# Performance work log

Hardware: AMD Instinct MI355X
Metric: run time of the kernel (lower is better)

## Reference

```python
import jax, jax.numpy as jnp
import numpy as np


def setup_inputs() -> dict:
    key = jax.random.key(0)
    k1, k2 = jax.random.split(key)
    shape = (64, 512, 512)  # batch of radar QPE grids
    # targets: rain rates uniform in [0, 100) so every weight bin is hit
    y = jax.random.uniform(k1, shape, dtype=jnp.float32) * 100.0
    # predictions: target plus noise -> realistic abs-diff magnitudes
    p = y + jax.random.normal(k2, shape, dtype=jnp.float32) * 5.0
    weights = jnp.array([0.1, 1.0, 2.0, 4.0, 8.0, 16.0, 32.0], dtype=jnp.float32)
    edge = jnp.array([0.0, 0.1, 10.0, 20.0, 30.0, 40.0, 50.0, 100.0], dtype=jnp.float32)
    return {"y": y, "p": p, "weights": weights, "edge": edge}


def reference(y, p, weights, edge):
    # diff = |p - y|
    diff = jnp.abs(p - y)
    # Fused bucketize replacing the 7-iteration mask+cat loop:
    # bin b satisfies edge[b] <= y < edge[b+1]  (searchsorted side='right' - 1)
    bin_idx = jnp.searchsorted(edge, y, side="right") - 1
    n_bins = weights.shape[0]
    valid = (bin_idx >= 0) & (bin_idx < n_bins)  # elements outside [edge[0], edge[-1]) are dropped
    w = jnp.where(valid, weights[jnp.clip(bin_idx, 0, n_bins - 1)], jnp.float32(0.0))
    total = jnp.sum(w * diff)
    count = jnp.sum(valid).astype(diff.dtype)  # len(loss_list) in the original
    return total / count
```

## Files before the change

kernel.cpp:

```cpp
#include <hip/hip_runtime.h>
#include <hip/hip_bf16.h>
#include <math.h>


#define MAXB 8
#define NBLOCKS 1024
#define BLOCK 256

__global__ __launch_bounds__(BLOCK) void wmae_partial(
    const float* __restrict__ y, const float* __restrict__ p,
    const float* __restrict__ weights, const float* __restrict__ edge,
    int n, int n_bins, int n_edges,
    float* __restrict__ psum, float* __restrict__ pcnt)
{
    __shared__ float sh_e[256];
    __shared__ float sh_w[256];
    for (int j = threadIdx.x; j < n_edges && j < 256; j += BLOCK) sh_e[j] = edge[j];
    for (int j = threadIdx.x; j < n_bins  && j < 256; j += BLOCK) sh_w[j] = weights[j];
    __syncthreads();

    float ev[MAXB], wv[MAXB];
#pragma unroll
    for (int j = 0; j < MAXB; ++j) {
        ev[j] = (j < n_edges) ? edge[j] : 3.4e38f;
        wv[j] = (j < n_bins)  ? weights[j] : 0.0f;
    }
    const float e0 = edge[0];
    const float eup = (n_bins < n_edges) ? edge[n_bins] : 3.4e38f;

    float sum = 0.0f;
    int   cnt = 0;

    auto proc = [&](float yy, float pp) {
        float w = 0.0f;
#pragma unroll
        for (int j = 0; j < MAXB; ++j) {
            if (j < n_bins) w = (yy >= ev[j]) ? wv[j] : w;
        }
        if (n_bins > MAXB) {
            for (int j = MAXB; j < n_bins; ++j)
                w = (yy >= sh_e[j]) ? sh_w[j] : w;
        }
        bool valid = (yy >= e0) && (yy < eup);
        sum += (valid ? w : 0.0f) * fabsf(pp - yy);
        cnt += valid ? 1 : 0;
    };

    const int tid    = blockIdx.x * BLOCK + threadIdx.x;
    const int stride = gridDim.x * BLOCK;
    const int n4     = n >> 2;
    const float4* y4 = (const float4*)y;
    const float4* p4 = (const float4*)p;

    for (int i = tid; i < n4; i += stride) {
        float4 yv = y4[i];
        float4 pv = p4[i];
        proc(yv.x, pv.x);
        proc(yv.y, pv.y);
        proc(yv.z, pv.z);
        proc(yv.w, pv.w);
    }
    for (int i = (n4 << 2) + tid; i < n; i += stride) proc(y[i], p[i]);

#pragma unroll
    for (int off = 32; off > 0; off >>= 1) {
        sum += __shfl_down(sum, off, 64);
        cnt += __shfl_down(cnt, off, 64);
    }
    __shared__ float wsum[BLOCK / 64];
    __shared__ int   wcnt[BLOCK / 64];
    const int wave = threadIdx.x >> 6;
    const int lane = threadIdx.x & 63;
    if (lane == 0) { wsum[wave] = sum; wcnt[wave] = cnt; }
    __syncthreads();
    if (threadIdx.x == 0) {
        float s = 0.0f; int c = 0;
#pragma unroll
        for (int w2 = 0; w2 < BLOCK / 64; ++w2) { s += wsum[w2]; c += wcnt[w2]; }
        psum[blockIdx.x] = s;
        pcnt[blockIdx.x] = (float)c;
    }
}

__global__ __launch_bounds__(BLOCK) void wmae_final(
    const float* __restrict__ psum, const float* __restrict__ pcnt,
    int nparts, float* __restrict__ out)
{
    float s = 0.0f, c = 0.0f;
    for (int i = threadIdx.x; i < nparts; i += BLOCK) { s += psum[i]; c += pcnt[i]; }
#pragma unroll
    for (int off = 32; off > 0; off >>= 1) {
        s += __shfl_down(s, off, 64);
        c += __shfl_down(c, off, 64);
    }
    __shared__ float wsum[BLOCK / 64];
    __shared__ float wcnt[BLOCK / 64];
    const int wave = threadIdx.x >> 6;
    const int lane = threadIdx.x & 63;
    if (lane == 0) { wsum[wave] = s; wcnt[wave] = c; }
    __syncthreads();
    if (threadIdx.x == 0) {
        float S = 0.0f, C = 0.0f;
#pragma unroll
        for (int w2 = 0; w2 < BLOCK / 64; ++w2) { S += wsum[w2]; C += wcnt[w2]; }
        out[0] = S / C;
    }
}

extern "C" void kernel_launch(void* const* d_in, const int* in_sizes, int n_in,
                              void* d_out, int out_size, void* d_ws, size_t ws_size,
                              hipStream_t stream) {
    const float* y       = (const float*)d_in[0];
    const float* p       = (const float*)d_in[1];
    const float* weights = (const float*)d_in[2];
    const float* edge    = (const float*)d_in[3];
    const int n       = in_sizes[0];
    const int n_bins  = in_sizes[2];
    const int n_edges = in_sizes[3];

    float* psum = (float*)d_ws;
    float* pcnt = psum + NBLOCKS;
    float* out  = (float*)d_out;

    wmae_partial<<<NBLOCKS, BLOCK, 0, stream>>>(y, p, weights, edge,
                                                n, n_bins, n_edges, psum, pcnt);
    wmae_final<<<1, BLOCK, 0, stream>>>(psum, pcnt, NBLOCKS, out);
}
```

Before: 148.7 us.

## Double-buffer per-wave chunk loads with inline asm and scalar-register bin tables

Replaces the grid-stride float4 loop with per-wave 4KB chunks loaded through inline-asm global_load_dwordx4, double-buffered so the next chunk's loads are in flight while the current one is computed, using explicit s_waitcnt. Edge and weight tables are forced into scalar registers via readfirstlane, the shared-memory copy is removed, and the bin loop no longer tests n_bins inside. The aim is more memory-level parallelism for this bandwidth-bound reduction. In exchange it doubles the live vector registers per thread and relies on hand-written waitcnt correctness.

After: 151.2 us. Within noise of the previous version (+1.7%).

```diff
diff --git a/kernel.cpp b/kernel.cpp
--- a/kernel.cpp
+++ b/kernel.cpp
@@ -4,8 +4,35 @@
 
 
 #define MAXB 8
-#define NBLOCKS 1024
+#define NB   1024
 #define BLOCK 256
+
+typedef float vf4 __attribute__((ext_vector_type(4)));
+
+__device__ __forceinline__ float to_sgpr(float x) {
+    return __uint_as_float(__builtin_amdgcn_readfirstlane(__float_as_uint(x)));
+}
+
+#define ISSUE(Y0,Y1,Y2,Y3,P0,P1,P2,P3, YB, PB)                                      \
+    asm volatile("global_load_dwordx4 %0, %1, off"             : "=v"(Y0) : "v"(YB)); \
+    asm volatile("global_load_dwordx4 %0, %1, off offset:1024" : "=v"(Y1) : "v"(YB)); \
+    asm volatile("global_load_dwordx4 %0, %1, off offset:2048" : "=v"(Y2) : "v"(YB)); \
+    asm volatile("global_load_dwordx4 %0, %1, off offset:3072" : "=v"(Y3) : "v"(YB)); \
+    asm volatile("global_load_dwordx4 %0, %1, off"             : "=v"(P0) : "v"(PB)); \
+    asm volatile("global_load_dwordx4 %0, %1, off offset:1024" : "=v"(P1) : "v"(PB)); \
+    asm volatile("global_load_dwordx4 %0, %1, off offset:2048" : "=v"(P2) : "v"(PB)); \
+    asm volatile("global_load_dwordx4 %0, %1, off offset:3072" : "=v"(P3) : "v"(PB));
+
+#define WAITN(N, Y0,Y1,Y2,Y3,P0,P1,P2,P3)                                           \
+    asm volatile("s_waitcnt vmcnt(" #N ")"                                          \
+        : "+v"(Y0), "+v"(Y1), "+v"(Y2), "+v"(Y3),                                   \
+          "+v"(P0), "+v"(P1), "+v"(P2), "+v"(P3) :: "memory");
+
+#define COMPUTE(Y0,Y1,Y2,Y3,P0,P1,P2,P3)                                            \
+    proc(Y0.x,P0.x); proc(Y0.y,P0.y); proc(Y0.z,P0.z); proc(Y0.w,P0.w);             \
+    proc(Y1.x,P1.x); proc(Y1.y,P1.y); proc(Y1.z,P1.z); proc(Y1.w,P1.w);             \
+    proc(Y2.x,P2.x); proc(Y2.y,P2.y); proc(Y2.z,P2.z); proc(Y2.w,P2.w);             \
+    proc(Y3.x,P3.x); proc(Y3.y,P3.y); proc(Y3.z,P3.z); proc(Y3.w,P3.w);
 
 __global__ __launch_bounds__(BLOCK) void wmae_partial(
     const float* __restrict__ y, const float* __restrict__ p,
@@ -13,20 +40,14 @@
     int n, int n_bins, int n_edges,
     float* __restrict__ psum, float* __restrict__ pcnt)
 {
-    __shared__ float sh_e[256];
-    __shared__ float sh_w[256];
-    for (int j = threadIdx.x; j < n_edges && j < 256; j += BLOCK) sh_e[j] = edge[j];
-    for (int j = threadIdx.x; j < n_bins  && j < 256; j += BLOCK) sh_w[j] = weights[j];
-    __syncthreads();
-
     float ev[MAXB], wv[MAXB];
 #pragma unroll
     for (int j = 0; j < MAXB; ++j) {
-        ev[j] = (j < n_edges) ? edge[j] : 3.4e38f;
-        wv[j] = (j < n_bins)  ? weights[j] : 0.0f;
+        ev[j] = to_sgpr((j < n_bins && j < n_edges) ? edge[j] : 3.4e38f);
+        wv[j] = to_sgpr((j < n_bins) ? weights[j] : 0.0f);
     }
-    const float e0 = edge[0];
-    const float eup = (n_bins < n_edges) ? edge[n_bins] : 3.4e38f;
+    const float e0  = to_sgpr(edge[0]);
+    const float eup = to_sgpr((n_bins < n_edges) ? edge[n_bins] : 3.4e38f);
 
     float sum = 0.0f;
     int   cnt = 0;
@@ -34,33 +55,70 @@
     auto proc = [&](float yy, float pp) {
         float w = 0.0f;
 #pragma unroll
-        for (int j = 0; j < MAXB; ++j) {
-            if (j < n_bins) w = (yy >= ev[j]) ? wv[j] : w;
-        }
-        if (n_bins > MAXB) {
-            for (int j = MAXB; j < n_bins; ++j)
-                w = (yy >= sh_e[j]) ? sh_w[j] : w;
-        }
+        for (int j = 0; j < MAXB; ++j) w = (yy >= ev[j]) ? wv[j] : w;
         bool valid = (yy >= e0) && (yy < eup);
         sum += (valid ? w : 0.0f) * fabsf(pp - yy);
         cnt += valid ? 1 : 0;
     };
 
-    const int tid    = blockIdx.x * BLOCK + threadIdx.x;
-    const int stride = gridDim.x * BLOCK;
-    const int n4     = n >> 2;
-    const float4* y4 = (const float4*)y;
-    const float4* p4 = (const float4*)p;
+    const int lane   = threadIdx.x & 63;
+    const int wid    = blockIdx.x * (BLOCK / 64) + (threadIdx.x >> 6);
+    const int nwaves = gridDim.x * (BLOCK / 64);
 
-    for (int i = tid; i < n4; i += stride) {
-        float4 yv = y4[i];
-        float4 pv = p4[i];
-        proc(yv.x, pv.x);
-        proc(yv.y, pv.y);
-        proc(yv.z, pv.z);
-        proc(yv.w, pv.w);
+    if (n_bins <= MAXB) {
+        const int nchunk = n >> 10;
+        int c = wid;
+        if (c < nchunk) {
+            vf4 ya0, ya1, ya2, ya3, pa0, pa1, pa2, pa3;
+            vf4 yb0, yb1, yb2, yb3, pb0, pb1, pb2, pb3;
+            {
+                const float* yb_ = y + ((size_t)c << 10) + lane * 4;
+                const float* pb_ = p + ((size_t)c << 10) + lane * 4;
+                ISSUE(ya0,ya1,ya2,ya3,pa0,pa1,pa2,pa3, yb_, pb_)
+            }
+            for (;;) {
+                int c2 = c + nwaves;
+                bool more = (c2 < nchunk);
+                if (more) {
+                    const float* yb_ = y + ((size_t)c2 << 10) + lane * 4;
+                    const float* pb_ = p + ((size_t)c2 << 10) + lane * 4;
+                    ISSUE(yb0,yb1,yb2,yb3,pb0,pb1,pb2,pb3, yb_, pb_)
+                    WAITN(8, ya0,ya1,ya2,ya3,pa0,pa1,pa2,pa3)
+                } else {
+                    WAITN(0, ya0,ya1,ya2,ya3,pa0,pa1,pa2,pa3)
+                }
+                COMPUTE(ya0,ya1,ya2,ya3,pa0,pa1,pa2,pa3)
+                if (!more) break;
+
+                int c3 = c2 + nwaves;
+                bool more2 = (c3 < nchunk);
+                if (more2) {
+                    const float* yb_ = y + ((size_t)c3 << 10) + lane * 4;
+                    const float* pb_ = p + ((size_t)c3 << 10) + lane * 4;
+                    ISSUE(ya0,ya1,ya2,ya3,pa0,pa1,pa2,pa3, yb_, pb_)
+                    WAITN(8, yb0,yb1,yb2,yb3,pb0,pb1,pb2,pb3)
+                } else {
+                    WAITN(0, yb0,yb1,yb2,yb3,pb0,pb1,pb2,pb3)
+                }
+                COMPUTE(yb0,yb1,yb2,yb3,pb0,pb1,pb2,pb3)
+                if (!more2) break;
+                c = c3;
+            }
+        }
+        const int n1  = nchunk << 10;
+        const int tid = blockIdx.x * BLOCK + threadIdx.x;
+        for (int k = n1 + tid; k < n; k += gridDim.x * BLOCK) proc(y[k], p[k]);
+    } else {
+        const int tid = blockIdx.x * BLOCK + threadIdx.x;
+        for (int k = tid; k < n; k += gridDim.x * BLOCK) {
+            float yy = y[k], pp = p[k];
+            float w = 0.0f;
+            for (int j = 0; j < n_bins; ++j) w = (yy >= edge[j]) ? weights[j] : w;
+            bool valid = (yy >= edge[0]) && (n_bins < n_edges ? (yy < edge[n_bins]) : true);
+            sum += (valid ? w : 0.0f) * fabsf(pp - yy);
+            cnt += valid ? 1 : 0;
+        }
     }
-    for (int i = (n4 << 2) + tid; i < n; i += stride) proc(y[i], p[i]);
 
 #pragma unroll
     for (int off = 32; off > 0; off >>= 1) {
@@ -70,7 +128,6 @@
     __shared__ float wsum[BLOCK / 64];
     __shared__ int   wcnt[BLOCK / 64];
     const int wave = threadIdx.x >> 6;
-    const int lane = threadIdx.x & 63;
     if (lane == 0) { wsum[wave] = sum; wcnt[wave] = cnt; }
     __syncthreads();
     if (threadIdx.x == 0) {
@@ -119,10 +176,10 @@
     const int n_edges = in_sizes[3];
 
     float* psum = (float*)d_ws;
-    float* pcnt = psum + NBLOCKS;
+    float* pcnt = psum + NB;
     float* out  = (float*)d_out;
 
-    wmae_partial<<<NBLOCKS, BLOCK, 0, stream>>>(y, p, weights, edge,
-                                                n, n_bins, n_edges, psum, pcnt);
-    wmae_final<<<1, BLOCK, 0, stream>>>(psum, pcnt, NBLOCKS, out);
+    wmae_partial<<<NB, BLOCK, 0, stream>>>(y, p, weights, edge,
+                                           n, n_bins, n_edges, psum, pcnt);
+    wmae_final<<<1, BLOCK, 0, stream>>>(psum, pcnt, NB, out);
 }
```
